# Performance work log

Hardware: AMD Instinct MI355X
Metric: run time of the kernel (lower is better)

The kernel has to match this reference:

```python
import jax, jax.numpy as jnp
import numpy as np

HEADS = 4
HEAD_DIM = 24
FOLD = 2   # fold_w = fold_h = fold_d
PROP = 2   # proposal_w = proposal_h = proposal_d


def _conv1x1(x, w, b):
    # x: [B,Cin,W,H,D], w: [Cout,Cin] -> [B,Cout,W,H,D]  (1x1x1 Conv3d)
    return jnp.einsum('bcwhd,oc->bowhd', x, w) + b[None, :, None, None, None]


def _fold(t, f):
    # 'b c (f1 w)(f2 h)(f3 d) -> (b f1 f2 f3) c w h d'
    b, c, W, H, D = t.shape
    w, h, d = W // f, H // f, D // f
    t = t.reshape(b, c, f, w, f, h, f, d)
    t = t.transpose(0, 2, 4, 6, 1, 3, 5, 7)
    return t.reshape(b * f * f * f, c, w, h, d)


def _unfold(t, f):
    # '(b f1 f2 f3) c w h d -> b c (f1 w)(f2 h)(f3 d)'
    bf, c, w, h, d = t.shape
    b = bf // (f * f * f)
    t = t.reshape(b, f, f, f, c, w, h, d)
    t = t.transpose(0, 4, 1, 5, 2, 6, 3, 7)
    return t.reshape(b, c, f * w, f * h, f * d)


def _adaptive_pool(t, p):
    # AdaptiveAvgPool3d((p,p,p)) with divisible spatial dims == block mean
    b, c, W, H, D = t.shape
    t = t.reshape(b, c, p, W // p, p, H // p, p, D // p)
    return t.mean(axis=(3, 5, 7))


def _normalize(v, eps=1e-12):
    n = jnp.linalg.norm(v, axis=-1, keepdims=True)
    return v / jnp.maximum(n, eps)


def setup_inputs() -> dict:
    key = jax.random.key(0)
    ks = jax.random.split(key, 4)
    B, C, W = 4, 96, 32
    inner = HEADS * HEAD_DIM  # 96
    return {
        'x': jax.random.normal(ks[0], (B, C, W, W, W), jnp.float32),
        'f_w': jax.random.normal(ks[1], (inner, C), jnp.float32) * 0.02,
        'f_b': jnp.zeros((inner,), jnp.float32),
        'v_w': jax.random.normal(ks[2], (inner, C), jnp.float32) * 0.02,
        'v_b': jnp.zeros((inner,), jnp.float32),
        'proj_w': jax.random.normal(ks[3], (C, inner), jnp.float32) * 0.02,
        'proj_b': jnp.zeros((C,), jnp.float32),
        'sim_alpha': jnp.ones((1,), jnp.float32),
        'sim_beta': jnp.zeros((1,), jnp.float32),
    }


def reference(x, f_w, f_b, v_w, v_b, proj_w, proj_b, sim_alpha, sim_beta):
    value = _conv1x1(x, v_w, v_b)
    feat = _conv1x1(x, f_w, f_b)

    def split_heads(t):  # 'b (e c) whd -> (b e) c whd'
        b, C = t.shape[:2]
        return t.reshape(b * HEADS, C // HEADS, *t.shape[2:])

    feat = split_heads(feat)
    value = split_heads(value)
    feat = _fold(feat, FOLD)
    value = _fold(value, FOLD)

    b, c, w, h, d = feat.shape
    N = w * h * d
    M = PROP ** 3
    centers = _adaptive_pool(feat, PROP)  # [b,c,p,p,p]
    value_centers = _adaptive_pool(value, PROP).reshape(b, c, M).transpose(0, 2, 1)  # [b,M,c]

    cflat = centers.reshape(b, c, M).transpose(0, 2, 1)  # [b,M,c]
    xflat = feat.reshape(b, c, N).transpose(0, 2, 1)     # [b,N,c]
    sim = jax.nn.sigmoid(sim_beta + sim_alpha *
                         jnp.einsum('bmc,bnc->bmn', _normalize(cflat), _normalize(xflat)))  # [b,M,N]
    idx = jnp.argmax(sim, axis=1)  # [b,N] hard assignment (first max, like torch)
    mask = (jnp.arange(M)[None, :, None] == idx[:, None, :]).astype(sim.dtype)
    sim = sim * mask

    value2 = value.reshape(b, c, N).transpose(0, 2, 1)  # [b,N,c]
    agg = (jnp.einsum('bmn,bnc->bmc', sim, value2) + value_centers) / (sim.sum(-1, keepdims=True) + 1.0)
    out = jnp.einsum('bmc,bmn->bnc', agg, sim)  # dispatch back to points
    out = out.transpose(0, 2, 1).reshape(b, c, w, h, d)

    out = _unfold(out, FOLD)
    bb = out.shape[0] // HEADS  # '(b e) c -> b (e c)'
    out = out.reshape(bb, HEADS * c, *out.shape[2:])
    out = _conv1x1(out, proj_w, proj_b)
    return out
```

## Files before the change

kernel.cpp:

```cpp
#include <hip/hip_runtime.h>
#include <hip/hip_bf16.h>


__global__ __launch_bounds__(256) void k0_prep(
    const float* __restrict__ fw, const float* __restrict__ pw,
    float* __restrict__ wfT, float* __restrict__ wpT)
{
    int t = blockIdx.x * 256 + threadIdx.x;
    if (t < 96 * 96) {
        int o = t / 96, c = t % 96;
        wfT[c * 96 + o] = fw[o * 96 + c];
        wpT[c * 96 + o] = pw[o * 96 + c];
    }
}

__global__ __launch_bounds__(256) void k_pool(
    const float* __restrict__ x, double* __restrict__ xmeanD)
{
    int gid = blockIdx.x * 256 + threadIdx.x;
    int bc = gid >> 6;
    int b = bc / 96, c = bc - b * 96;
    int fm = gid & 63;
    int f1 = (fm >> 5) & 1, f2 = (fm >> 4) & 1, f3 = (fm >> 3) & 1, m = fm & 7;
    int W0 = f1 * 16 + (m >> 2) * 8;
    int H0 = f2 * 16 + ((m >> 1) & 1) * 8;
    int D0 = f3 * 16 + (m & 1) * 8;
    const float* xb = x + ((size_t)b * 96 + c) * 32768;
    double s = 0.0;
    for (int iw = 0; iw < 8; ++iw)
        for (int ih = 0; ih < 8; ++ih) {
            const float4* p = (const float4*)(xb + (W0 + iw) * 1024 + (H0 + ih) * 32 + D0);
            float4 a = p[0], q = p[1];
            s += (double)a.x + (double)a.y + (double)a.z + (double)a.w
               + (double)q.x + (double)q.y + (double)q.z + (double)q.w;
        }
    xmeanD[(size_t)(b * 64 + fm) * 96 + c] = s * (1.0 / 512.0);
}

__global__ __launch_bounds__(192) void k_cent(
    const float* __restrict__ fw, const float* __restrict__ fb,
    const float* __restrict__ vw, const float* __restrict__ vb,
    const double* __restrict__ xmeanD, double* __restrict__ chat,
    float* __restrict__ vcent)
{
    __shared__ double centL[8][24];
    __shared__ double dnv[8];
    const int B2 = blockIdx.x, t = threadIdx.x;
    const int mm = t / 24, co = t - mm * 24;
    const int b = B2 >> 5, g = (B2 >> 3) & 3, fff = B2 & 7;
    const int ob = g * 24;
    const double* xm = xmeanD + (size_t)(b * 64 + fff * 8 + mm) * 96;
    double cF = (double)fb[ob + co];
    float  cV = vb[ob + co];
    const float* fr = fw + (ob + co) * 96;
    const float* vr = vw + (ob + co) * 96;
    for (int ci = 0; ci < 96; ++ci) {
        double xv = xm[ci];
        cF += (double)fr[ci] * xv;
        cV += vr[ci] * (float)xv;
    }
    centL[mm][co] = cF;
    __syncthreads();
    if (t < 8) {
        double ss = 0.0;
        #pragma unroll
        for (int cc = 0; cc < 24; ++cc) ss += centL[t][cc] * centL[t][cc];
        dnv[t] = fmax(sqrt(ss), 1e-12);
    }
    __syncthreads();
    chat[(size_t)B2 * 192 + mm * 24 + co] = cF / dnv[mm];
    vcent[(size_t)B2 * 192 + t] = cV;
}

__global__ __launch_bounds__(256) void k_prep_u(
    const float* __restrict__ fw, const float* __restrict__ fb,
    const double* __restrict__ chat, double* __restrict__ uG)
{
    int gid = blockIdx.x * 256 + threadIdx.x;
    if (gid >= 128 * 776) return;
    int B2 = gid / 776, rem = gid - B2 * 776;
    int m = rem / 97, c = rem - m * 97;
    int g = (B2 >> 3) & 3;
    const double* ch = chat + (size_t)B2 * 192 + m * 24;
    double s = 0.0;
    if (c < 96) {
        for (int o = 0; o < 24; ++o) s += (double)fw[(g * 24 + o) * 96 + c] * ch[o];
    } else {
        for (int o = 0; o < 24; ++o) s += (double)fb[g * 24 + o] * ch[o];
    }
    uG[gid] = s;
}

__global__ __launch_bounds__(256) void k1_conv(
    const float* __restrict__ x, const float* __restrict__ wfT,
    const float* __restrict__ fb, const double* __restrict__ uG,
    const float* __restrict__ al, const float* __restrict__ be,
    float* __restrict__ svb, unsigned char* __restrict__ bmb)
{
    __shared__ float xt[96][64];
    __shared__ double u_l[4][776];
    const int tile = blockIdx.x;
    const int b = tile >> 9;
    const int r = tile & 511;
    const int W = r >> 4;
    const int Hq = (r >> 1) & 7;
    const int f3 = r & 1;
    const int f1 = W >> 4, f2 = Hq >> 2;
    const float* xb = x + (size_t)b * 96 * 32768 + W * 1024 + Hq * 4 * 32 + f3 * 16;

    #pragma unroll
    for (int k = 0; k < 24; ++k) {
        int idx = k * 256 + threadIdx.x;
        int c = idx >> 6, i2 = idx & 63;
        xt[c][i2] = xb[(size_t)c * 32768 + (i2 >> 4) * 32 + (i2 & 15)];
    }
    #pragma unroll
    for (int g = 0; g < 4; ++g) {
        int B2g = (b << 5) | (g << 3) | (f1 << 2) | (f2 << 1) | f3;
        for (int k = threadIdx.x; k < 776; k += 256)
            u_l[g][k] = uG[(size_t)B2g * 776 + k];
    }
    __syncthreads();

    const int i = threadIdx.x & 63;
    const int g = threadIdx.x >> 6;
    const int ob = __builtin_amdgcn_readfirstlane(g * 24);
    const double* ug = u_l[g];

    double a[8];
    #pragma unroll
    for (int m = 0; m < 8; ++m) a[m] = ug[m * 97 + 96];
    float accN[24];
    #pragma unroll
    for (int oo = 0; oo < 24; ++oo) accN[oo] = fb[ob + oo];

    for (int c = 0; c < 96; ++c) {
        const float xv = xt[c][i];
        const double xd = (double)xv;
        #pragma unroll
        for (int m = 0; m < 8; ++m) a[m] = fma(xd, ug[m * 97 + c], a[m]);
        const float* wr = wfT + c * 96 + ob;
        #pragma unroll
        for (int oo = 0; oo < 24; ++oo) accN[oo] = fmaf(xv, wr[oo], accN[oo]);
    }

    float ss = 0.f;
    #pragma unroll
    for (int oo = 0; oo < 24; ++oo) ss = fmaf(accN[oo], accN[oo], ss);
    const float dn = fmaxf(sqrtf(ss), 1e-12f);

    const double alpha = (double)al[0];
    const double beta  = (double)be[0];
    int bm = 0; double dbest = a[0];
    if (alpha > 0.0) {
        #pragma unroll
        for (int m = 1; m < 8; ++m) if (a[m] > dbest) { dbest = a[m]; bm = m; }
    } else if (alpha < 0.0) {
        #pragma unroll
        for (int m = 1; m < 8; ++m) if (a[m] < dbest) { dbest = a[m]; bm = m; }
    }
    const double tv = beta + alpha * (dbest / (double)dn);
    const float sv = 1.f / (1.f + expf(-(float)tv));

    const int n = ((W & 15) << 8) | (((Hq & 3) * 4 + (i >> 4)) << 4) | (i & 15);
    const int B2 = (b << 5) | (g << 3) | (f1 << 2) | (f2 << 1) | f3;
    svb[(size_t)B2 * 4096 + n] = sv;
    bmb[(size_t)B2 * 4096 + n] = (unsigned char)bm;
}

__global__ __launch_bounds__(256) void k_xagg(
    const float* __restrict__ x, const float* __restrict__ svb,
    const unsigned char* __restrict__ bmb, float* __restrict__ xagg,
    float* __restrict__ cntb)
{
    __shared__ float red[256][33];
    __shared__ float red2[8][32];
    const int grp = blockIdx.x / 97;
    const int c   = blockIdx.x - grp * 97;
    const int b = grp >> 3, fff = grp & 7;
    const int f1 = fff >> 2, f2 = (fff >> 1) & 1, f3 = fff & 1;
    const int t = threadIdx.x;
    const float* xc = x + ((size_t)b * 96 + (c < 96 ? c : 0)) * 32768;
    const int sbase = f1 * 16 * 1024 + f2 * 16 * 32 + f3 * 16;

    float acc[4][8];
    #pragma unroll
    for (int g = 0; g < 4; ++g)
        #pragma unroll
        for (int m = 0; m < 8; ++m) acc[g][m] = 0.f;

    #pragma unroll 4
    for (int k = 0; k < 16; ++k) {
        const int n = k * 256 + t;
        const int s = sbase + (n >> 8) * 1024 + ((n >> 4) & 15) * 32 + (n & 15);
        const float xv = (c < 96) ? xc[s] : 1.0f;
        #pragma unroll
        for (int g = 0; g < 4; ++g) {
            const int B2g = (b << 5) | (g << 3) | fff;
            const float svv = svb[(size_t)B2g * 4096 + n];
            const int bmv = bmb[(size_t)B2g * 4096 + n];
            const float p = svv * xv;
            #pragma unroll
            for (int m = 0; m < 8; ++m)
                acc[g][m] += (bmv == m) ? p : 0.f;
        }
    }

    #pragma unroll
    for (int g = 0; g < 4; ++g)
        #pragma unroll
        for (int m = 0; m < 8; ++m) red[t][g * 8 + m] = acc[g][m];
    __syncthreads();
    {
        const int j = t & 31, part = t >> 5;
        float s = 0.f;
        #pragma unroll
        for (int kk = 0; kk < 32; ++kk) s += red[part * 32 + kk][j];
        red2[part][j] = s;
    }
    __syncthreads();
    if (t < 32) {
        float s = 0.f;
        #pragma unroll
        for (int p = 0; p < 8; ++p) s += red2[p][t];
        const int g = t >> 3, m = t & 7;
        const int B2g = (b << 5) | (g << 3) | fff;
        if (c < 96) xagg[((size_t)B2g * 8 + m) * 96 + c] = s;
        else        cntb[B2g * 8 + m] = s;
    }
}

__global__ __launch_bounds__(192) void k_sums(
    const float* __restrict__ vw, const float* __restrict__ vb,
    const float* __restrict__ xagg, const float* __restrict__ cntb,
    float* __restrict__ sums)
{
    const int B2 = blockIdx.x, t = threadIdx.x;
    const int m = t / 24, co = t - m * 24;
    const int g = (B2 >> 3) & 3;
    const float* xa = xagg + ((size_t)B2 * 8 + m) * 96;
    const float* vr = vw + (g * 24 + co) * 96;
    float s = 0.f;
    for (int ci = 0; ci < 96; ++ci) s = fmaf(vr[ci], xa[ci], s);
    sums[(size_t)B2 * 192 + t] = s + cntb[B2 * 8 + m] * vb[g * 24 + co];
}

__global__ __launch_bounds__(256) void k_disp(
    const float* __restrict__ sums, const float* __restrict__ cnt,
    const float* __restrict__ vcent, const float* __restrict__ svb,
    const unsigned char* __restrict__ bmb, const float* __restrict__ wpT,
    const float* __restrict__ pb, float* __restrict__ out)
{
    __shared__ float xt[96][64];
    __shared__ float agg_l[8][8][24];
    const int tile = blockIdx.x;
    const int b = tile >> 9;
    const int s0 = (tile & 511) << 6;
    const int f1 = (s0 >> 14) & 1, f2 = (s0 >> 9) & 1;
    for (int k = threadIdx.x; k < 1536; k += 256) {
        int slot = k / 192, rem = k - slot * 192;
        int g = slot >> 1, f3 = slot & 1;
        int B2 = (b << 5) | (g << 3) | (f1 << 2) | (f2 << 1) | f3;
        int mm = rem / 24;
        ((float*)agg_l)[k] =
            (sums[(size_t)B2 * 192 + rem] + vcent[(size_t)B2 * 192 + rem]) /
            (cnt[B2 * 8 + mm] + 1.f);
    }
    __syncthreads();

    const int i = threadIdx.x & 63;
    const int g = threadIdx.x >> 6;
    const int s = s0 + i;
    const int D = s & 31, H = (s >> 5) & 31, W = s >> 10;
    const int f3 = D >> 4;
    const int n = ((W & 15) << 8) | ((H & 15) << 4) | (D & 15);
    const int B2 = (b << 5) | (g << 3) | (f1 << 2) | (f2 << 1) | f3;
    const int slot = (g << 1) | f3;
    const float svv = svb[(size_t)B2 * 4096 + n];
    const int bmv = bmb[(size_t)B2 * 4096 + n];
    #pragma unroll
    for (int c = 0; c < 24; ++c) xt[g * 24 + c][i] = svv * agg_l[slot][bmv][c];
    __syncthreads();

    const int ob = __builtin_amdgcn_readfirstlane(g * 24);
    float acc[24];
    #pragma unroll
    for (int oo = 0; oo < 24; ++oo) acc[oo] = pb[ob + oo];
    for (int c = 0; c < 96; ++c) {
        float xv = xt[c][i];
        const float* wr = wpT + c * 96 + ob;
        #pragma unroll
        for (int oo = 0; oo < 24; ++oo) acc[oo] = fmaf(wr[oo], xv, acc[oo]);
    }
    #pragma unroll
    for (int oo = 0; oo < 24; ++oo)
        out[((size_t)b * 96 + ob + oo) * 32768 + s0 + i] = acc[oo];
}

extern "C" void kernel_launch(void* const* d_in, const int* in_sizes, int n_in,
                              void* d_out, int out_size, void* d_ws, size_t ws_size,
                              hipStream_t stream)
{
    const float* x  = (const float*)d_in[0];
    const float* fw = (const float*)d_in[1];
    const float* fb = (const float*)d_in[2];
    const float* vw = (const float*)d_in[3];
    const float* vb = (const float*)d_in[4];
    const float* pw = (const float*)d_in[5];
    const float* pb = (const float*)d_in[6];
    const float* al = (const float*)d_in[7];
    const float* be = (const float*)d_in[8];
    float* out = (float*)d_out;

    char* ws = (char*)d_ws;
    float*  wfT   = (float*)(ws);
    float*  wpT   = (float*)(ws + 36864);
    double* xmeanD= (double*)(ws + 73728);
    double* chat  = (double*)(ws + 270336);
    double* uG    = (double*)(ws + 466944);
    float*  vcent = (float*)(ws + 1261568);
    float*  sums  = (float*)(ws + 1359872);
    float*  xagg  = (float*)(ws + 1458176);
    float*  cntb  = (float*)(ws + 1851392);
    float*  svb   = (float*)(ws + 1855488);
    unsigned char* bmb = (unsigned char*)(ws + 3952640);

    k0_prep<<<36, 256, 0, stream>>>(fw, pw, wfT, wpT);
    k_pool<<<96, 256, 0, stream>>>(x, xmeanD);
    k_cent<<<128, 192, 0, stream>>>(fw, fb, vw, vb, xmeanD, chat, vcent);
    k_prep_u<<<388, 256, 0, stream>>>(fw, fb, chat, uG);
    k1_conv<<<2048, 256, 0, stream>>>(x, wfT, fb, uG, al, be, svb, bmb);
    k_xagg<<<3104, 256, 0, stream>>>(x, svb, bmb, xagg, cntb);
    k_sums<<<128, 192, 0, stream>>>(vw, vb, xagg, cntb, sums);
    k_disp<<<2048, 256, 0, stream>>>(sums, cntb, vcent, svb, bmb, wpT, pb, out);
}
```

Measured before the change: 283.6 us.

## Fold projection into per-cluster aggregates and stream uG from global memory

The output projection is moved algebraically onto the 8 cluster aggregates per group: a new k_pagg kernel computes proj_w·agg per cluster, so k_disp only does a gather, scale and sum over 4 heads instead of a full 96x96 per-point matmul. This removes most of the FLOPs and the LDS transpose in the dispatch stage. k1_conv also drops its 4x776 double LDS staging of uG and reads uG directly through wave-uniform (scalar) loads, with uG relaid out as [c][m]. The cost is an extra small kernel and a changed access pattern on uG that relies on scalar-cache hits.

```diff
diff --git a/kernel.cpp b/kernel.cpp
--- a/kernel.cpp
+++ b/kernel.cpp
@@ -3,13 +3,15 @@
 
 
 __global__ __launch_bounds__(256) void k0_prep(
-    const float* __restrict__ fw, const float* __restrict__ pw,
-    float* __restrict__ wfT, float* __restrict__ wpT)
+    const float* __restrict__ fw, const float* __restrict__ vw,
+    const float* __restrict__ pw, float* __restrict__ wfT,
+    float* __restrict__ wvT, float* __restrict__ wpT)
 {
     int t = blockIdx.x * 256 + threadIdx.x;
     if (t < 96 * 96) {
         int o = t / 96, c = t % 96;
         wfT[c * 96 + o] = fw[o * 96 + c];
+        wvT[c * 96 + o] = vw[o * 96 + c];
         wpT[c * 96 + o] = pw[o * 96 + c];
     }
 }
@@ -79,7 +81,7 @@
     int gid = blockIdx.x * 256 + threadIdx.x;
     if (gid >= 128 * 776) return;
     int B2 = gid / 776, rem = gid - B2 * 776;
-    int m = rem / 97, c = rem - m * 97;
+    int c = rem >> 3, m = rem & 7;
     int g = (B2 >> 3) & 3;
     const double* ch = chat + (size_t)B2 * 192 + m * 24;
     double s = 0.0;
@@ -88,7 +90,7 @@
     } else {
         for (int o = 0; o < 24; ++o) s += (double)fb[g * 24 + o] * ch[o];
     }
-    uG[gid] = s;
+    uG[(size_t)B2 * 776 + c * 8 + m] = s;
 }
 
 __global__ __launch_bounds__(256) void k1_conv(
@@ -98,7 +100,6 @@
     float* __restrict__ svb, unsigned char* __restrict__ bmb)
 {
     __shared__ float xt[96][64];
-    __shared__ double u_l[4][776];
     const int tile = blockIdx.x;
     const int b = tile >> 9;
     const int r = tile & 511;
@@ -114,22 +115,18 @@
         int c = idx >> 6, i2 = idx & 63;
         xt[c][i2] = xb[(size_t)c * 32768 + (i2 >> 4) * 32 + (i2 & 15)];
     }
-    #pragma unroll
-    for (int g = 0; g < 4; ++g) {
-        int B2g = (b << 5) | (g << 3) | (f1 << 2) | (f2 << 1) | f3;
-        for (int k = threadIdx.x; k < 776; k += 256)
-            u_l[g][k] = uG[(size_t)B2g * 776 + k];
-    }
     __syncthreads();
 
     const int i = threadIdx.x & 63;
     const int g = threadIdx.x >> 6;
     const int ob = __builtin_amdgcn_readfirstlane(g * 24);
-    const double* ug = u_l[g];
+    const int B2 = (b << 5) | (g << 3) | (f1 << 2) | (f2 << 1) | f3;
+    const int uoff = __builtin_amdgcn_readfirstlane(B2 * 776);
+    const double* ug = uG + uoff;
 
     double a[8];
     #pragma unroll
-    for (int m = 0; m < 8; ++m) a[m] = ug[m * 97 + 96];
+    for (int m = 0; m < 8; ++m) a[m] = ug[768 + m];
     float accN[24];
     #pragma unroll
     for (int oo = 0; oo < 24; ++oo) accN[oo] = fb[ob + oo];
@@ -137,8 +134,9 @@
     for (int c = 0; c < 96; ++c) {
         const float xv = xt[c][i];
         const double xd = (double)xv;
-        #pragma unroll
-        for (int m = 0; m < 8; ++m) a[m] = fma(xd, ug[m * 97 + c], a[m]);
+        const double* uc = ug + c * 8;
+        #pragma unroll
+        for (int m = 0; m < 8; ++m) a[m] = fma(xd, uc[m], a[m]);
         const float* wr = wfT + c * 96 + ob;
         #pragma unroll
         for (int oo = 0; oo < 24; ++oo) accN[oo] = fmaf(xv, wr[oo], accN[oo]);
@@ -163,7 +161,6 @@
     const float sv = 1.f / (1.f + expf(-(float)tv));
 
     const int n = ((W & 15) << 8) | (((Hq & 3) * 4 + (i >> 4)) << 4) | (i & 15);
-    const int B2 = (b << 5) | (g << 3) | (f1 << 2) | (f2 << 1) | f3;
     svb[(size_t)B2 * 4096 + n] = sv;
     bmb[(size_t)B2 * 4096 + n] = (unsigned char)bm;
 }
@@ -230,71 +227,91 @@
     }
 }
 
-__global__ __launch_bounds__(192) void k_sums(
-    const float* __restrict__ vw, const float* __restrict__ vb,
-    const float* __restrict__ xagg, const float* __restrict__ cntb,
-    float* __restrict__ sums)
-{
+__global__ __launch_bounds__(256) void k_pagg(
+    const float* __restrict__ wvT, const float* __restrict__ vb,
+    const float* __restrict__ wpT, const float* __restrict__ xagg,
+    const float* __restrict__ cntb, const float* __restrict__ vcent,
+    float* __restrict__ pagg)
+{
+    __shared__ float xa_l[8][96];
+    __shared__ float agg_l[8][25];
+    __shared__ float cnt_l[8];
     const int B2 = blockIdx.x, t = threadIdx.x;
-    const int m = t / 24, co = t - m * 24;
     const int g = (B2 >> 3) & 3;
-    const float* xa = xagg + ((size_t)B2 * 8 + m) * 96;
-    const float* vr = vw + (g * 24 + co) * 96;
-    float s = 0.f;
-    for (int ci = 0; ci < 96; ++ci) s = fmaf(vr[ci], xa[ci], s);
-    sums[(size_t)B2 * 192 + t] = s + cntb[B2 * 8 + m] * vb[g * 24 + co];
+    for (int k = t; k < 768; k += 256) ((float*)xa_l)[k] = xagg[(size_t)B2 * 768 + k];
+    if (t < 8) cnt_l[t] = cntb[B2 * 8 + t];
+    __syncthreads();
+    if (t < 192) {
+        const int m = t / 24, o = t - m * 24;
+        float s = 0.f;
+        for (int ci = 0; ci < 96; ++ci)
+            s = fmaf(wvT[ci * 96 + g * 24 + o], xa_l[m][ci], s);
+        s += cnt_l[m] * vb[g * 24 + o] + vcent[(size_t)B2 * 192 + t];
+        agg_l[m][o] = s / (cnt_l[m] + 1.f);
+    }
+    __syncthreads();
+    #pragma unroll
+    for (int r = 0; r < 3; ++r) {
+        const int k = r * 256 + t;
+        const int m = k / 96, C = k - m * 96;
+        float s = 0.f;
+        #pragma unroll
+        for (int o = 0; o < 24; ++o)
+            s = fmaf(wpT[(g * 24 + o) * 96 + C], agg_l[m][o], s);
+        pagg[(size_t)B2 * 768 + k] = s;
+    }
 }
 
 __global__ __launch_bounds__(256) void k_disp(
-    const float* __restrict__ sums, const float* __restrict__ cnt,
-    const float* __restrict__ vcent, const float* __restrict__ svb,
-    const unsigned char* __restrict__ bmb, const float* __restrict__ wpT,
-    const float* __restrict__ pb, float* __restrict__ out)
-{
-    __shared__ float xt[96][64];
-    __shared__ float agg_l[8][8][24];
+    const float* __restrict__ pagg, const float* __restrict__ svb,
+    const unsigned char* __restrict__ bmb, const float* __restrict__ pb,
+    float* __restrict__ out)
+{
+    __shared__ float pagg_l[4][776];
+    __shared__ float svs[4][64];
+    __shared__ unsigned char bms[4][64];
     const int tile = blockIdx.x;
     const int b = tile >> 9;
-    const int s0 = (tile & 511) << 6;
-    const int f1 = (s0 >> 14) & 1, f2 = (s0 >> 9) & 1;
-    for (int k = threadIdx.x; k < 1536; k += 256) {
-        int slot = k / 192, rem = k - slot * 192;
-        int g = slot >> 1, f3 = slot & 1;
-        int B2 = (b << 5) | (g << 3) | (f1 << 2) | (f2 << 1) | f3;
-        int mm = rem / 24;
-        ((float*)agg_l)[k] =
-            (sums[(size_t)B2 * 192 + rem] + vcent[(size_t)B2 * 192 + rem]) /
-            (cnt[B2 * 8 + mm] + 1.f);
-    }
-    __syncthreads();
-
-    const int i = threadIdx.x & 63;
-    const int g = threadIdx.x >> 6;
-    const int s = s0 + i;
-    const int D = s & 31, H = (s >> 5) & 31, W = s >> 10;
-    const int f3 = D >> 4;
-    const int n = ((W & 15) << 8) | ((H & 15) << 4) | (D & 15);
-    const int B2 = (b << 5) | (g << 3) | (f1 << 2) | (f2 << 1) | f3;
-    const int slot = (g << 1) | f3;
-    const float svv = svb[(size_t)B2 * 4096 + n];
-    const int bmv = bmb[(size_t)B2 * 4096 + n];
-    #pragma unroll
-    for (int c = 0; c < 24; ++c) xt[g * 24 + c][i] = svv * agg_l[slot][bmv][c];
-    __syncthreads();
-
-    const int ob = __builtin_amdgcn_readfirstlane(g * 24);
+    const int r = tile & 511;
+    const int W = r >> 4;
+    const int Hq = (r >> 1) & 7;
+    const int f3 = r & 1;
+    const int f1 = W >> 4, f2 = Hq >> 2;
+    const int t = threadIdx.x;
+    const int i = t & 63, q = t >> 6;
+
+    const int n = ((W & 15) << 8) | ((((Hq & 3) << 2) | (i >> 4)) << 4) | (i & 15);
+    {
+        const int B2q = (b << 5) | (q << 3) | (f1 << 2) | (f2 << 1) | f3;
+        svs[q][i] = svb[(size_t)B2q * 4096 + n];
+        bms[q][i] = bmb[(size_t)B2q * 4096 + n];
+    }
+    for (int k = t; k < 3072; k += 256) {
+        const int g = k >> 10;
+        const int gg = k / 768, rem = k - gg * 768;
+        const int m = rem / 96, c = rem - m * 96;
+        const int B2g = (b << 5) | (gg << 3) | (f1 << 2) | (f2 << 1) | f3;
+        (void)g;
+        pagg_l[gg][m * 97 + c] = pagg[(size_t)B2g * 768 + rem];
+    }
+    __syncthreads();
+
+    const int co = q * 24;
     float acc[24];
     #pragma unroll
-    for (int oo = 0; oo < 24; ++oo) acc[oo] = pb[ob + oo];
-    for (int c = 0; c < 96; ++c) {
-        float xv = xt[c][i];
-        const float* wr = wpT + c * 96 + ob;
-        #pragma unroll
-        for (int oo = 0; oo < 24; ++oo) acc[oo] = fmaf(wr[oo], xv, acc[oo]);
-    }
+    for (int oo = 0; oo < 24; ++oo) acc[oo] = pb[co + oo];
+    #pragma unroll
+    for (int g = 0; g < 4; ++g) {
+        const float sv = svs[g][i];
+        const int bm = bms[g][i];
+        const float* pg = &pagg_l[g][bm * 97 + co];
+        #pragma unroll
+        for (int oo = 0; oo < 24; ++oo) acc[oo] = fmaf(sv, pg[oo], acc[oo]);
+    }
+    const int s = W * 1024 + ((Hq << 2) | (i >> 4)) * 32 + f3 * 16 + (i & 15);
     #pragma unroll
     for (int oo = 0; oo < 24; ++oo)
-        out[((size_t)b * 96 + ob + oo) * 32768 + s0 + i] = acc[oo];
+        out[((size_t)b * 96 + co + oo) * 32768 + s] = acc[oo];
 }
 
 extern "C" void kernel_launch(void* const* d_in, const int* in_sizes, int n_in,
@@ -315,22 +332,23 @@
     char* ws = (char*)d_ws;
     float*  wfT   = (float*)(ws);
     float*  wpT   = (float*)(ws + 36864);
-    double* xmeanD= (double*)(ws + 73728);
-    double* chat  = (double*)(ws + 270336);
-    double* uG    = (double*)(ws + 466944);
-    float*  vcent = (float*)(ws + 1261568);
-    float*  sums  = (float*)(ws + 1359872);
-    float*  xagg  = (float*)(ws + 1458176);
-    float*  cntb  = (float*)(ws + 1851392);
-    float*  svb   = (float*)(ws + 1855488);
-    unsigned char* bmb = (unsigned char*)(ws + 3952640);
-
-    k0_prep<<<36, 256, 0, stream>>>(fw, pw, wfT, wpT);
+    float*  wvT   = (float*)(ws + 73728);
+    double* xmeanD= (double*)(ws + 110592);
+    double* chat  = (double*)(ws + 307200);
+    double* uG    = (double*)(ws + 503808);
+    float*  vcent = (float*)(ws + 1298432);
+    float*  xagg  = (float*)(ws + 1396736);
+    float*  cntb  = (float*)(ws + 1789952);
+    float*  pagg  = (float*)(ws + 1794048);
+    float*  svb   = (float*)(ws + 2187264);
+    unsigned char* bmb = (unsigned char*)(ws + 4284416);
+
+    k0_prep<<<36, 256, 0, stream>>>(fw, vw, pw, wfT, wvT, wpT);
     k_pool<<<96, 256, 0, stream>>>(x, xmeanD);
     k_cent<<<128, 192, 0, stream>>>(fw, fb, vw, vb, xmeanD, chat, vcent);
     k_prep_u<<<388, 256, 0, stream>>>(fw, fb, chat, uG);
     k1_conv<<<2048, 256, 0, stream>>>(x, wfT, fb, uG, al, be, svb, bmb);
     k_xagg<<<3104, 256, 0, stream>>>(x, svb, bmb, xagg, cntb);
-    k_sums<<<128, 192, 0, stream>>>(vw, vb, xagg, cntb, sums);
-    k_disp<<<2048, 256, 0, stream>>>(sums, cntb, vcent, svb, bmb, wpT, pb, out);
-}
+    k_pagg<<<128, 256, 0, stream>>>(wvT, vb, wpT, xagg, cntb, vcent, pagg);
+    k_disp<<<2048, 256, 0, stream>>>(pagg, svb, bmb, pb, out);
+}
```

Result: faster. 248.8 us (-12.3%).
